# Kernel tuning notes

Measured on AMD Instinct MI355X. Metric: run time of the kernel, lower is better.

The kernel has to match this reference:

```python
import jax, jax.numpy as jnp
import numpy as np

B, T, F_IN, S_IN = 32, 4096, 1024, 1024
D, H = 1024, 16
DEPTH = D // H  # 64


def setup_inputs() -> dict:
    key = jax.random.key(0)
    ks = jax.random.split(key, 8)
    scale = lambda fan_in: 1.0 / np.sqrt(fan_in)
    return {
        "features": jax.random.normal(ks[0], (B, T, F_IN), dtype=jnp.float32),
        "state": jax.random.normal(ks[1], (B, S_IN), dtype=jnp.float32),
        "Wq": jax.random.normal(ks[2], (S_IN, D), dtype=jnp.float32) * scale(S_IN),
        "bq": jnp.zeros((D,), dtype=jnp.float32),
        "Wv": jax.random.normal(ks[3], (F_IN, D), dtype=jnp.float32) * scale(F_IN),
        "bv": jnp.zeros((D,), dtype=jnp.float32),
        "Wd": jax.random.normal(ks[4], (D, D), dtype=jnp.float32) * scale(D),
        "bd": jnp.zeros((D,), dtype=jnp.float32),
    }


def reference(features, state, Wq, bq, Wv, bv, Wd, bd):
    # state is concatenated (single tensor -> identity) and given a time axis of 1
    q = state[:, None, :] @ Wq + bq              # [B, 1, D]
    v = features @ Wv + bv                       # [B, T, D]
    # split heads: [B, H, q_len, depth]
    qh = q.reshape(B, 1, H, DEPTH).transpose(0, 2, 1, 3)   # [B, H, 1, depth]
    vh = v.reshape(B, T, H, DEPTH).transpose(0, 2, 1, 3)   # [B, H, T, depth]
    # scaled dot-product attention, key == value, no mask
    logits = jnp.einsum('bhqd,bhkd->bhqk', qh, vh) / jnp.sqrt(jnp.float32(DEPTH))
    attn = jax.nn.softmax(logits, axis=-1)                 # [B, H, 1, T]
    out = jnp.einsum('bhqk,bhkd->bhqd', attn, vh)          # [B, H, 1, depth]
    # merge heads back: [B, 1, D]
    out = out.transpose(0, 2, 1, 3).reshape(B, 1, D)
    # GlobalAveragePooling1D over the (length-1) time axis
    pooled = out.mean(axis=1)                              # [B, D]
    return pooled @ Wd + bd                                # [B, D]
```

## Files before the change

### kernel.cpp

```cpp
#include <hip/hip_runtime.h>
#include <hip/hip_bf16.h>
#include <math.h>

#define BB 32
#define TT 4096
#define FF 1024
#define DD 1024
#define HH 16
#define DEPTH 64
#define CHUNKS 16
#define TC 256


__global__ __launch_bounds__(256) void smallgemm(const float* __restrict__ X,
                                                 const float* __restrict__ W,
                                                 const float* __restrict__ bias,
                                                 float* __restrict__ Y) {
    const int b = blockIdx.y;
    const int n = blockIdx.x * 128 + (threadIdx.x & 31) * 4;
    const int kg = threadIdx.x >> 5;
    const float* __restrict__ x = X + b * DD + kg * 128;
    float4 acc = make_float4(0.f, 0.f, 0.f, 0.f);
#pragma unroll 4
    for (int k = 0; k < 128; ++k) {
        const float s = x[k];
        const float4 wr = *reinterpret_cast<const float4*>(W + (size_t)(kg * 128 + k) * DD + n);
        acc.x = fmaf(s, wr.x, acc.x);
        acc.y = fmaf(s, wr.y, acc.y);
        acc.z = fmaf(s, wr.z, acc.z);
        acc.w = fmaf(s, wr.w, acc.w);
    }
    __shared__ float4 red[8][33];
    red[kg][threadIdx.x & 31] = acc;
    __syncthreads();
    if (threadIdx.x < 32) {
        float4 r = red[0][threadIdx.x];
#pragma unroll
        for (int g = 1; g < 8; ++g) {
            const float4 p = red[g][threadIdx.x];
            r.x += p.x; r.y += p.y; r.z += p.z; r.w += p.w;
        }
        const int nn = blockIdx.x * 128 + threadIdx.x * 4;
        const float4 bb = *reinterpret_cast<const float4*>(bias + nn);
        r.x += bb.x; r.y += bb.y; r.z += bb.z; r.w += bb.w;
        *reinterpret_cast<float4*>(Y + b * DD + nn) = r;
    }
}

__global__ __launch_bounds__(512) void ckern(const float* __restrict__ q,
                                             const float* __restrict__ bv,
                                             float* __restrict__ c) {
    const int tid = threadIdx.x;
    const int b = tid >> 4, h = tid & 15;
    float s = 0.f;
#pragma unroll
    for (int d = 0; d < DEPTH; ++d)
        s = fmaf(bv[h * DEPTH + d], q[b * DD + h * DEPTH + d], s);
    c[tid] = s;
}

__global__ __launch_bounds__(256) void ukern(const float* __restrict__ Wv,
                                             const float* __restrict__ q,
                                             float* __restrict__ u) {
    const int h = blockIdx.x;
    const int f0 = blockIdx.y * 64;
    __shared__ float qs[BB][DEPTH];
    __shared__ float wvs[DEPTH][DEPTH + 1];
    const int tid = threadIdx.x;
#pragma unroll
    for (int i = 0; i < 8; ++i) {
        const int idx = i * 256 + tid;
        const int bq_ = idx >> 6, d = idx & 63;
        qs[bq_][d] = q[bq_ * DD + h * DEPTH + d];
    }
#pragma unroll
    for (int i = 0; i < 16; ++i) {
        const int idx = i * 256 + tid;
        const int r = idx >> 6, d = idx & 63;
        wvs[r][d] = Wv[(size_t)(f0 + r) * DD + h * DEPTH + d];
    }
    __syncthreads();
    const int fl = tid & 63;
    const int bg = (tid >> 6) * 8;
    float acc[8] = {0.f, 0.f, 0.f, 0.f, 0.f, 0.f, 0.f, 0.f};
#pragma unroll 8
    for (int d = 0; d < 64; ++d) {
        const float wv = wvs[fl][d];
#pragma unroll
        for (int j = 0; j < 8; ++j) acc[j] = fmaf(wv, qs[bg + j][d], acc[j]);
    }
#pragma unroll
    for (int j = 0; j < 8; ++j)
        u[((size_t)(bg + j) * HH + h) * FF + f0 + fl] = acc[j];
}

__global__ __launch_bounds__(256) void attnfused(const float* __restrict__ feat,
                                                 const float* __restrict__ u,
                                                 const float* __restrict__ c,
                                                 float* __restrict__ wpart,
                                                 float* __restrict__ mpart,
                                                 float* __restrict__ spart) {
    const int b = blockIdx.y;
    const int chunk = blockIdx.x;
    const int t0 = chunk * TC;
    __shared__ float fs[TC][36];
    __shared__ float us[HH][32];
    __shared__ float ls[TC][20];
    __shared__ float red[HH][17];
    __shared__ float msh[HH];
    const int tid = threadIdx.x;
    const int tx = tid & 63;
    const int h0 = (tid >> 6) * 4;
    const int r0 = tid >> 3;
    const int f4 = (tid & 7) * 4;

    float acc[4][4] = {};
    for (int fc = 0; fc < 32; ++fc) {
        const int f0 = fc * 32;
        __syncthreads();
#pragma unroll
        for (int i = 0; i < 8; ++i) {
            const int row = r0 + i * 32;
            const float4 v = *reinterpret_cast<const float4*>(
                feat + (size_t)(b * TT + t0 + row) * FF + f0 + f4);
            *reinterpret_cast<float4*>(&fs[row][f4]) = v;
        }
        if (tid < 128) {
            const int h = tid >> 3;
            const float4 v = *reinterpret_cast<const float4*>(
                u + (size_t)(b * HH + h) * FF + f0 + f4);
            *reinterpret_cast<float4*>(&us[h][f4]) = v;
        }
        __syncthreads();
#pragma unroll
        for (int g = 0; g < 8; ++g) {
            float4 uu[4];
#pragma unroll
            for (int j = 0; j < 4; ++j)
                uu[j] = *reinterpret_cast<const float4*>(&us[h0 + j][g * 4]);
#pragma unroll
            for (int k = 0; k < 4; ++k) {
                const float4 a = *reinterpret_cast<const float4*>(&fs[tx + k * 64][g * 4]);
#pragma unroll
                for (int j = 0; j < 4; ++j) {
                    acc[k][j] = fmaf(a.x, uu[j].x, acc[k][j]);
                    acc[k][j] = fmaf(a.y, uu[j].y, acc[k][j]);
                    acc[k][j] = fmaf(a.z, uu[j].z, acc[k][j]);
                    acc[k][j] = fmaf(a.w, uu[j].w, acc[k][j]);
                }
            }
        }
    }
    __syncthreads();
#pragma unroll
    for (int j = 0; j < 4; ++j) {
        const float cc = c[b * HH + h0 + j];
#pragma unroll
        for (int k = 0; k < 4; ++k)
            ls[tx + k * 64][h0 + j] = (acc[k][j] + cc) * 0.125f;
    }
    __syncthreads();

    const int hh = tid >> 4, ii = tid & 15;
    float mx = -1e30f;
#pragma unroll
    for (int k = 0; k < 16; ++k) mx = fmaxf(mx, ls[ii + k * 16][hh]);
    red[hh][ii] = mx;
    __syncthreads();
    if (tid < HH) {
        float m = red[tid][0];
#pragma unroll
        for (int i = 1; i < 16; ++i) m = fmaxf(m, red[tid][i]);
        msh[tid] = m;
    }
    __syncthreads();
    const float m = msh[hh];
    float sm = 0.f;
#pragma unroll
    for (int k = 0; k < 16; ++k) {
        const int t = ii + k * 16;
        const float p = __expf(ls[t][hh] - m);
        ls[t][hh] = p;
        sm += p;
    }
    red[hh][ii] = sm;
    __syncthreads();
    if (tid < HH) {
        float s = 0.f;
#pragma unroll
        for (int i = 0; i < 16; ++i) s += red[tid][i];
        mpart[(b * CHUNKS + chunk) * HH + tid] = msh[tid];
        spart[(b * CHUNKS + chunk) * HH + tid] = s;
    }
    __syncthreads();

    const int f = tid * 4;
    float4 wacc[16];
#pragma unroll
    for (int h = 0; h < 16; ++h) wacc[h] = make_float4(0.f, 0.f, 0.f, 0.f);
    const float* __restrict__ fb = feat + (size_t)(b * TT + t0) * FF + f;
#pragma unroll 4
    for (int t = 0; t < TC; ++t) {
        const float4 x = *reinterpret_cast<const float4*>(fb + (size_t)t * FF);
#pragma unroll
        for (int j = 0; j < 4; ++j) {
            const float4 p4 = *reinterpret_cast<const float4*>(&ls[t][j * 4]);
            wacc[j * 4 + 0].x = fmaf(p4.x, x.x, wacc[j * 4 + 0].x);
            wacc[j * 4 + 0].y = fmaf(p4.x, x.y, wacc[j * 4 + 0].y);
            wacc[j * 4 + 0].z = fmaf(p4.x, x.z, wacc[j * 4 + 0].z);
            wacc[j * 4 + 0].w = fmaf(p4.x, x.w, wacc[j * 4 + 0].w);
            wacc[j * 4 + 1].x = fmaf(p4.y, x.x, wacc[j * 4 + 1].x);
            wacc[j * 4 + 1].y = fmaf(p4.y, x.y, wacc[j * 4 + 1].y);
            wacc[j * 4 + 1].z = fmaf(p4.y, x.z, wacc[j * 4 + 1].z);
            wacc[j * 4 + 1].w = fmaf(p4.y, x.w, wacc[j * 4 + 1].w);
            wacc[j * 4 + 2].x = fmaf(p4.z, x.x, wacc[j * 4 + 2].x);
            wacc[j * 4 + 2].y = fmaf(p4.z, x.y, wacc[j * 4 + 2].y);
            wacc[j * 4 + 2].z = fmaf(p4.z, x.z, wacc[j * 4 + 2].z);
            wacc[j * 4 + 2].w = fmaf(p4.z, x.w, wacc[j * 4 + 2].w);
            wacc[j * 4 + 3].x = fmaf(p4.w, x.x, wacc[j * 4 + 3].x);
            wacc[j * 4 + 3].y = fmaf(p4.w, x.y, wacc[j * 4 + 3].y);
            wacc[j * 4 + 3].z = fmaf(p4.w, x.z, wacc[j * 4 + 3].z);
            wacc[j * 4 + 3].w = fmaf(p4.w, x.w, wacc[j * 4 + 3].w);
        }
    }
    float* __restrict__ wp = wpart + ((size_t)(b * CHUNKS + chunk) * HH) * FF + f;
#pragma unroll
    for (int h = 0; h < 16; ++h)
        *reinterpret_cast<float4*>(wp + (size_t)h * FF) = wacc[h];
}

__global__ __launch_bounds__(256) void outkern(const float* __restrict__ wpart,
                                               const float* __restrict__ mpart,
                                               const float* __restrict__ spart,
                                               const float* __restrict__ Wv,
                                               const float* __restrict__ bv,
                                               float* __restrict__ pooled) {
    const int bh = blockIdx.x;
    const int b = bh >> 4, h = bh & 15;
    const int tid = threadIdx.x;
    __shared__ float ws_[FF];
    __shared__ float mtmp[CHUNKS], stmp[CHUNKS];
    if (tid < CHUNKS) {
        mtmp[tid] = mpart[(b * CHUNKS + tid) * HH + h];
        stmp[tid] = spart[(b * CHUNKS + tid) * HH + h];
    }
    __syncthreads();
    float M = -1e30f;
#pragma unroll
    for (int cc = 0; cc < CHUNKS; ++cc) M = fmaxf(M, mtmp[cc]);
    float Z = 0.f;
    float coef[CHUNKS];
#pragma unroll
    for (int cc = 0; cc < CHUNKS; ++cc) {
        coef[cc] = __expf(mtmp[cc] - M);
        Z = fmaf(stmp[cc], coef[cc], Z);
    }
    const float zinv = 1.f / Z;
#pragma unroll
    for (int i = 0; i < 4; ++i) {
        const int f_ = i * 256 + tid;
        float s = 0.f;
#pragma unroll 4
        for (int cc = 0; cc < CHUNKS; ++cc)
            s = fmaf(wpart[((size_t)(b * CHUNKS + cc) * HH + h) * FF + f_], coef[cc], s);
        ws_[f_] = s * zinv;
    }
    __syncthreads();
    const int dd = tid & 63;
    const int fq = tid >> 6;
    float acc = 0.f;
#pragma unroll 8
    for (int i = 0; i < 256; ++i) {
        const int f_ = fq * 256 + i;
        acc = fmaf(ws_[f_], Wv[(size_t)f_ * DD + h * DEPTH + dd], acc);
    }
    __shared__ float part[4][64];
    part[fq][dd] = acc;
    __syncthreads();
    if (tid < 64) {
        const float r = part[0][dd] + part[1][dd] + part[2][dd] + part[3][dd];
        pooled[b * DD + h * DEPTH + dd] = r + bv[h * DEPTH + dd];
    }
}

extern "C" void kernel_launch(void* const* d_in, const int* in_sizes, int n_in,
                              void* d_out, int out_size, void* d_ws, size_t ws_size,
                              hipStream_t stream) {
    const float* feat  = (const float*)d_in[0];
    const float* state = (const float*)d_in[1];
    const float* Wq    = (const float*)d_in[2];
    const float* bq    = (const float*)d_in[3];
    const float* Wv    = (const float*)d_in[4];
    const float* bv    = (const float*)d_in[5];
    const float* Wd    = (const float*)d_in[6];
    const float* bd    = (const float*)d_in[7];
    float* out = (float*)d_out;
    float* ws = (float*)d_ws;

    float* q      = ws;
    float* c      = ws + 32768;
    float* u      = ws + 33280;
    float* mpart  = ws + 557568;
    float* spart  = ws + 565760;
    float* wpart  = ws + 573952;
    float* pooled = ws + 8962560;

    smallgemm<<<dim3(8, BB), 256, 0, stream>>>(state, Wq, bq, q);
    ckern<<<1, 512, 0, stream>>>(q, bv, c);
    ukern<<<dim3(HH, FF / 64), 256, 0, stream>>>(Wv, q, u);
    attnfused<<<dim3(CHUNKS, BB), 256, 0, stream>>>(feat, u, c, wpart, mpart, spart);
    outkern<<<BB * HH, 256, 0, stream>>>(wpart, mpart, spart, Wv, bv, pooled);
    smallgemm<<<dim3(8, BB), 256, 0, stream>>>(pooled, Wd, bd, out);
}
```

Baseline: 903.8 us.

## Double attnfused block size to 512 threads and alias shared memory buffers

The fused attention kernel now runs 512 threads per block. Each thread computes half as many logits, and the weighted-sum pass over features covers two columns instead of four, which halves the accumulator registers. Shared memory is packed into one aliased buffer (fs with ls, us with red) so that several blocks fit per CU under launch_bounds(512,4). The goal is more resident waves to hide the latency of streaming features from HBM. In exchange there are more threads per barrier and narrower float2 global loads.

```diff
diff --git a/kernel.cpp b/kernel.cpp
--- a/kernel.cpp
+++ b/kernel.cpp
@@ -94,33 +94,37 @@
         u[((size_t)(bg + j) * HH + h) * FF + f0 + fl] = acc[j];
 }
 
-__global__ __launch_bounds__(256) void attnfused(const float* __restrict__ feat,
-                                                 const float* __restrict__ u,
-                                                 const float* __restrict__ c,
-                                                 float* __restrict__ wpart,
-                                                 float* __restrict__ mpart,
-                                                 float* __restrict__ spart) {
+__global__ __launch_bounds__(512, 4) void attnfused(const float* __restrict__ feat,
+                                                    const float* __restrict__ u,
+                                                    const float* __restrict__ c,
+                                                    float* __restrict__ wpart,
+                                                    float* __restrict__ mpart,
+                                                    float* __restrict__ spart) {
     const int b = blockIdx.y;
     const int chunk = blockIdx.x;
     const int t0 = chunk * TC;
-    __shared__ float fs[TC][36];
-    __shared__ float us[HH][32];
-    __shared__ float ls[TC][20];
-    __shared__ float red[HH][17];
-    __shared__ float msh[HH];
+    __shared__ __align__(16) char smem[39040];
+    float (*fs)[36]  = reinterpret_cast<float(*)[36]>(smem);
+    float (*ls)[20]  = reinterpret_cast<float(*)[20]>(smem);
+    float (*us)[32]  = reinterpret_cast<float(*)[32]>(smem + 36864);
+    float (*red)[33] = reinterpret_cast<float(*)[33]>(smem + 36864);
+    float* msh       = reinterpret_cast<float*>(smem + 38976);
+
     const int tid = threadIdx.x;
     const int tx = tid & 63;
-    const int h0 = (tid >> 6) * 4;
+    const int wave = tid >> 6;
+    const int h0 = (wave & 3) * 4;
+    const int th = wave >> 2;
     const int r0 = tid >> 3;
     const int f4 = (tid & 7) * 4;
 
-    float acc[4][4] = {};
+    float acc[2][4] = {};
     for (int fc = 0; fc < 32; ++fc) {
         const int f0 = fc * 32;
         __syncthreads();
 #pragma unroll
-        for (int i = 0; i < 8; ++i) {
-            const int row = r0 + i * 32;
+        for (int i = 0; i < 4; ++i) {
+            const int row = r0 + i * 64;
             const float4 v = *reinterpret_cast<const float4*>(
                 feat + (size_t)(b * TT + t0 + row) * FF + f0 + f4);
             *reinterpret_cast<float4*>(&fs[row][f4]) = v;
@@ -139,8 +143,9 @@
             for (int j = 0; j < 4; ++j)
                 uu[j] = *reinterpret_cast<const float4*>(&us[h0 + j][g * 4]);
 #pragma unroll
-            for (int k = 0; k < 4; ++k) {
-                const float4 a = *reinterpret_cast<const float4*>(&fs[tx + k * 64][g * 4]);
+            for (int k = 0; k < 2; ++k) {
+                const float4 a = *reinterpret_cast<const float4*>(
+                    &fs[th * 128 + k * 64 + tx][g * 4]);
 #pragma unroll
                 for (int j = 0; j < 4; ++j) {
                     acc[k][j] = fmaf(a.x, uu[j].x, acc[k][j]);
@@ -156,29 +161,29 @@
     for (int j = 0; j < 4; ++j) {
         const float cc = c[b * HH + h0 + j];
 #pragma unroll
-        for (int k = 0; k < 4; ++k)
-            ls[tx + k * 64][h0 + j] = (acc[k][j] + cc) * 0.125f;
-    }
-    __syncthreads();
-
-    const int hh = tid >> 4, ii = tid & 15;
+        for (int k = 0; k < 2; ++k)
+            ls[th * 128 + k * 64 + tx][h0 + j] = (acc[k][j] + cc) * 0.125f;
+    }
+    __syncthreads();
+
+    const int hh = tid >> 5, ii = tid & 31;
     float mx = -1e30f;
 #pragma unroll
-    for (int k = 0; k < 16; ++k) mx = fmaxf(mx, ls[ii + k * 16][hh]);
+    for (int k = 0; k < 8; ++k) mx = fmaxf(mx, ls[ii + k * 32][hh]);
     red[hh][ii] = mx;
     __syncthreads();
     if (tid < HH) {
         float m = red[tid][0];
 #pragma unroll
-        for (int i = 1; i < 16; ++i) m = fmaxf(m, red[tid][i]);
+        for (int i = 1; i < 32; ++i) m = fmaxf(m, red[tid][i]);
         msh[tid] = m;
     }
     __syncthreads();
     const float m = msh[hh];
     float sm = 0.f;
 #pragma unroll
-    for (int k = 0; k < 16; ++k) {
-        const int t = ii + k * 16;
+    for (int k = 0; k < 8; ++k) {
+        const int t = ii + k * 32;
         const float p = __expf(ls[t][hh] - m);
         ls[t][hh] = p;
         sm += p;
@@ -188,45 +193,37 @@
     if (tid < HH) {
         float s = 0.f;
 #pragma unroll
-        for (int i = 0; i < 16; ++i) s += red[tid][i];
+        for (int i = 0; i < 32; ++i) s += red[tid][i];
         mpart[(b * CHUNKS + chunk) * HH + tid] = msh[tid];
         spart[(b * CHUNKS + chunk) * HH + tid] = s;
     }
     __syncthreads();
 
-    const int f = tid * 4;
-    float4 wacc[16];
-#pragma unroll
-    for (int h = 0; h < 16; ++h) wacc[h] = make_float4(0.f, 0.f, 0.f, 0.f);
+    const int f = tid * 2;
+    float2 wacc[16];
+#pragma unroll
+    for (int h = 0; h < 16; ++h) wacc[h] = make_float2(0.f, 0.f);
     const float* __restrict__ fb = feat + (size_t)(b * TT + t0) * FF + f;
-#pragma unroll 4
+#pragma unroll 8
     for (int t = 0; t < TC; ++t) {
-        const float4 x = *reinterpret_cast<const float4*>(fb + (size_t)t * FF);
+        const float2 x = *reinterpret_cast<const float2*>(fb + (size_t)t * FF);
 #pragma unroll
         for (int j = 0; j < 4; ++j) {
             const float4 p4 = *reinterpret_cast<const float4*>(&ls[t][j * 4]);
             wacc[j * 4 + 0].x = fmaf(p4.x, x.x, wacc[j * 4 + 0].x);
             wacc[j * 4 + 0].y = fmaf(p4.x, x.y, wacc[j * 4 + 0].y);
-            wacc[j * 4 + 0].z = fmaf(p4.x, x.z, wacc[j * 4 + 0].z);
-            wacc[j * 4 + 0].w = fmaf(p4.x, x.w, wacc[j * 4 + 0].w);
             wacc[j * 4 + 1].x = fmaf(p4.y, x.x, wacc[j * 4 + 1].x);
             wacc[j * 4 + 1].y = fmaf(p4.y, x.y, wacc[j * 4 + 1].y);
-            wacc[j * 4 + 1].z = fmaf(p4.y, x.z, wacc[j * 4 + 1].z);
-            wacc[j * 4 + 1].w = fmaf(p4.y, x.w, wacc[j * 4 + 1].w);
             wacc[j * 4 + 2].x = fmaf(p4.z, x.x, wacc[j * 4 + 2].x);
             wacc[j * 4 + 2].y = fmaf(p4.z, x.y, wacc[j * 4 + 2].y);
-            wacc[j * 4 + 2].z = fmaf(p4.z, x.z, wacc[j * 4 + 2].z);
-            wacc[j * 4 + 2].w = fmaf(p4.z, x.w, wacc[j * 4 + 2].w);
             wacc[j * 4 + 3].x = fmaf(p4.w, x.x, wacc[j * 4 + 3].x);
             wacc[j * 4 + 3].y = fmaf(p4.w, x.y, wacc[j * 4 + 3].y);
-            wacc[j * 4 + 3].z = fmaf(p4.w, x.z, wacc[j * 4 + 3].z);
-            wacc[j * 4 + 3].w = fmaf(p4.w, x.w, wacc[j * 4 + 3].w);
         }
     }
     float* __restrict__ wp = wpart + ((size_t)(b * CHUNKS + chunk) * HH) * FF + f;
 #pragma unroll
     for (int h = 0; h < 16; ++h)
-        *reinterpret_cast<float4*>(wp + (size_t)h * FF) = wacc[h];
+        *reinterpret_cast<float2*>(wp + (size_t)h * FF) = wacc[h];
 }
 
 __global__ __launch_bounds__(256) void outkern(const float* __restrict__ wpart,
@@ -308,7 +305,7 @@
     smallgemm<<<dim3(8, BB), 256, 0, stream>>>(state, Wq, bq, q);
     ckern<<<1, 512, 0, stream>>>(q, bv, c);
     ukern<<<dim3(HH, FF / 64), 256, 0, stream>>>(Wv, q, u);
-    attnfused<<<dim3(CHUNKS, BB), 256, 0, stream>>>(feat, u, c, wpart, mpart, spart);
+    attnfused<<<dim3(CHUNKS, BB), 512, 0, stream>>>(feat, u, c, wpart, mpart, spart);
     outkern<<<BB * HH, 256, 0, stream>>>(wpart, mpart, spart, Wv, bv, pooled);
     smallgemm<<<dim3(8, BB), 256, 0, stream>>>(pooled, Wd, bd, out);
 }
```

New measurement: 945.1 us. 1.05x slower.
